# Kernel optimization log

Hardware: AMD Instinct MI355X
Metric: run time of the kernel (lower is better)

## Reference

```python
import jax, jax.numpy as jnp
import numpy as np

B, C, H, W = 4, 128, 192, 192

def _conv(x, w, b, pad):
    y = jax.lax.conv_general_dilated(
        x, w, window_strides=(1, 1), padding=[(pad, pad), (pad, pad)],
        dimension_numbers=('NCHW', 'OIHW', 'NCHW'))
    return y + b[None, :, None, None]

def setup_inputs() -> dict:
    key = jax.random.key(0)
    ks = jax.random.split(key, 11)
    def he(k, shape):
        fan_in = shape[1] * shape[2] * shape[3]
        return jax.random.normal(k, shape, jnp.float32) * np.sqrt(2.0 / fan_in)
    return {
        'x':  jax.random.normal(ks[0], (B, C, H, W), jnp.float32),
        'w1': he(ks[1], (C // 2, C, 3, 3)),      'b1': jnp.zeros((C // 2,), jnp.float32),
        'w2': he(ks[2], (C // 4, C // 2, 3, 3)), 'b2': jnp.zeros((C // 4,), jnp.float32),
        'w3': he(ks[3], (9, C // 4, 1, 1)),      'b3': jnp.zeros((9,), jnp.float32),
        'f1': he(ks[4], (C, C, 3, 3)),           'fb1': jnp.zeros((C,), jnp.float32),
        'f2': he(ks[5], (C, C, 3, 3)),           'fb2': jnp.zeros((C,), jnp.float32),
    }

def reference(x, w1, b1, w2, b2, w3, b3, f1, fb1, f2, fb2):
    b, c, h, w = x.shape
    # kernel estimator: conv3x3 -> relu -> conv3x3 -> relu -> conv1x1 (9 logits)
    k = jax.nn.relu(_conv(x, w1, b1, 1))
    k = jax.nn.relu(_conv(k, w2, b2, 1))
    k = _conv(k, w3, b3, 0)                     # (b, 9, h, w)
    kernel = jax.nn.softmax(k, axis=1)[:, None]  # (b, 1, 9, h, w)
    # 3x3 neighborhoods (equivalent to F.unfold with padding=1), row-major taps
    xp = jnp.pad(x, ((0, 0), (0, 0), (1, 1), (1, 1)))
    patches = jnp.stack([xp[:, :, i:i + h, j:j + w]
                         for i in range(3) for j in range(3)], axis=2)  # (b, c, 9, h, w)
    out = jnp.sum(patches * kernel, axis=2)     # (b, c, h, w)
    # feature extract
    feats = jax.nn.relu(_conv(out, f1, fb1, 1))
    feats = _conv(feats, f2, fb2, 1)
    return feats
```

## Files before the change

### kernel.cpp

```cpp
#include <hip/hip_runtime.h>
#include <math.h>

#define BB 4
#define CC 128
#define HH 192
#define WW 192
#define HWSZ (HH * WW)
#define NPIX (BB * HWSZ)
#define PD 194

typedef __attribute__((ext_vector_type(8))) short short8;
typedef __attribute__((ext_vector_type(4))) short short4v;
typedef __attribute__((ext_vector_type(4))) float float4v;

__device__ __forceinline__ short f2bf(float f) {
    unsigned u = __float_as_uint(f);
    u += 0x7FFF + ((u >> 16) & 1);
    return (short)(u >> 16);
}
__device__ __forceinline__ float bf2f(short s) {
    return __uint_as_float(((unsigned)(unsigned short)s) << 16);
}

__global__ void prep_w_kernel(const float* __restrict__ w,
                              short* __restrict__ wp,
                              int CIN, int COUT, int total) {
    int idx = blockIdx.x * blockDim.x + threadIdx.x;
    if (idx >= total) return;
    int ci8 = idx & 7;
    int t   = idx >> 3;
    int co  = t % COUT;  t /= COUT;
    int lg  = t % 4;     t /= 4;
    int tap3 = t % 3;    t /= 3;
    int tt  = t % 3;
    int ck  = t / 3;
    int cin = ck * 32 + lg * 8 + ci8;
    int tap = tt * 3 + tap3;
    wp[idx] = f2bf(w[(co * CIN + cin) * 9 + tap]);
}

__global__ void zero_pads_kernel(short* __restrict__ p0,
                                 short* __restrict__ p1,
                                 short* __restrict__ p2) {
    int idx = blockIdx.x * blockDim.x + threadIdx.x;
    if (idx >= 3 * 64 * 772) return;
    int e   = idx % 772;
    int bc  = (idx / 772) % 64;
    int buf = idx / (772 * 64);
    short* base = (buf == 0) ? p0 : (buf == 1) ? p1 : p2;
    int row, col;
    if (e < 194)      { row = 0;   col = e; }
    else if (e < 388) { row = 193; col = e - 194; }
    else { int e2 = e - 388; row = 1 + (e2 >> 1); col = (e2 & 1) * 193; }
    short8 z = {0, 0, 0, 0, 0, 0, 0, 0};
    *(short8*)&base[(((size_t)bc * PD + row) * PD + col) * 8] = z;
}

__global__ void x_prep_kernel(const float* __restrict__ x,
                              short* __restrict__ xp) {
    int idx = blockIdx.x * blockDim.x + threadIdx.x;
    if (idx >= BB * 16 * HWSZ) return;
    int w  = idx % WW;
    int h  = (idx / WW) % HH;
    int cg = (idx / HWSZ) % 16;
    int b  = idx / (HWSZ * 16);
    const float* p = x + ((size_t)(b * CC + cg * 8) * HH + h) * WW + w;
    short8 pk;
#pragma unroll
    for (int j = 0; j < 8; ++j) pk[j] = f2bf(p[(size_t)j * HWSZ]);
    *(short8*)&xp[((((size_t)b * 16 + cg) * PD + h + 1) * PD + (w + 1)) * 8] = pk;
}

template <int CIN, int COUT, int WAVES_M, int WAVES_N, int WM, int WN,
          bool RELU, bool OUT_F32>
__global__ __launch_bounds__(WAVES_M * WAVES_N * 64, 4)
void conv3x3_wlds(const short* __restrict__ in,
                  const short* __restrict__ wp,
                  const float* __restrict__ bias,
                  void* __restrict__ outv) {
    constexpr int CKN   = CIN / 32;
    constexpr int CG_IN = CIN / 8;
    constexpr int CGO   = COUT / 8;
    constexpr int NT    = WAVES_M * WAVES_N * 64;
    constexpr int SUB   = 3 * 4 * COUT * 8;
    constexpr int SUBB  = SUB * 2;
    constexpr int ATS   = 4 * COUT * 16;
    constexpr int NS    = CKN * 3;
    constexpr int KTMAX = CKN * 9;
    constexpr int CKB   = PD * PD * 64;
    static_assert(WAVES_M * WM * 16 == COUT, "M tiling");
    static_assert(WAVES_N * WN * 16 == 192, "N tiling");

    __shared__ __align__(16) short s_w[2 * SUB];

    const int tid  = threadIdx.x;
    const int lin  = blockIdx.y * gridDim.x + blockIdx.x;
    const int L    = (lin & 7) * ((HH * BB) >> 3) + (lin >> 3);
    const int h    = L % HH;
    const int b    = L / HH;
    const int lane = tid & 63;
    const int wv   = tid >> 6;
    const int wv_m = wv % WAVES_M;
    const int wv_n = wv / WAVES_M;
    const int ln15 = lane & 15;
    const int lg   = lane >> 4;

    float4v acc[WM][WN];
#pragma unroll
    for (int mi = 0; mi < WM; ++mi)
#pragma unroll
        for (int ni = 0; ni < WN; ++ni)
            acc[mi][ni] = (float4v){0.f, 0.f, 0.f, 0.f};

    short8 Aa[2][WM], Bb[3][WN];

    const int colb = (wv_n * WN * 16 + ln15) * 16;
    const char* rowb0 = (const char*)(in +
        (((size_t)b * CG_IN + lg) * PD + h) * (size_t)PD * 8) + colb;
    const char* rowb1 = rowb0 + PD * 16;
    const char* rowb2 = rowb0 + 2 * PD * 16;

    const char* aBase = (const char*)&s_w[0] +
        lg * (COUT * 16) + (wv_m * WM) * 256 + ln15 * 16;

    auto loadBpf = [&](int dy, int dx, short8* dst) {
        const char* rp = (dy == 0) ? rowb0 : (dy == 1) ? rowb1 : rowb2;
#pragma unroll
        for (int ni = 0; ni < WN; ++ni)
            dst[ni] = *(const short8*)(rp + dx * 16 + ni * 256);
    };

    const short* wsrc = wp;
    int wpar = 0;
    auto stageIssue = [&]() {
        constexpr int UNITS = SUB / 8;
        short* dstb = &s_w[wpar * SUB];
#pragma unroll
        for (int u = 0; u < (UNITS + NT - 1) / NT; ++u) {
            int i = tid + u * NT;
            if (UNITS % NT == 0 || i < UNITS)
                __builtin_amdgcn_global_load_lds(
                    (const __attribute__((address_space(1))) void*)&wsrc[i * 8],
                    (__attribute__((address_space(3))) void*)&dstb[i * 8], 16, 0, 0);
        }
        asm volatile("" ::: "memory");
        wsrc += SUB;
        wpar ^= 1;
    };

    stageIssue();
    loadBpf(0, 0, Bb[0]);
    loadBpf(0, 1, Bb[1]);
    asm volatile("s_waitcnt vmcnt(6)" ::: "memory");
    __builtin_amdgcn_s_barrier();
    asm volatile("" ::: "memory");

    int par = 0;
    for (int ck = 0; ck < CKN; ++ck) {
#pragma unroll
        for (int tt = 0; tt < 3; ++tt) {
            const int s = ck * 3 + tt;
            const bool notLast = (s + 1 < NS);
            if (notLast) stageIssue();
            const char* aP = aBase + (par ? SUBB : 0);
#pragma unroll
            for (int mi = 0; mi < WM; ++mi)
                Aa[0][mi] = *(const short8*)(aP + mi * 256);
#pragma unroll
            for (int t3 = 0; t3 < 3; ++t3) {
                if (t3 < 2) {
#pragma unroll
                    for (int mi = 0; mi < WM; ++mi)
                        Aa[(t3 + 1) & 1][mi] =
                            *(const short8*)(aP + (t3 + 1) * ATS + mi * 256);
                }
                const int kt = s * 3 + t3;
                if (kt + 2 < KTMAX) {
                    const int tp = (tt * 3 + t3 + 2) % 9;
                    loadBpf(tp / 3, tp % 3, Bb[(t3 + 2) % 3]);
                }
#pragma unroll
                for (int mi = 0; mi < WM; ++mi)
#pragma unroll
                    for (int ni = 0; ni < WN; ++ni)
                        acc[mi][ni] = __builtin_amdgcn_mfma_f32_16x16x32_bf16(
                            Aa[t3 & 1][mi], Bb[t3][ni], acc[mi][ni], 0, 0, 0);
                if (tt == 2 && t3 == 0) {
                    rowb0 += CKB; rowb1 += CKB; rowb2 += CKB;
                }
            }
            if (notLast) {
                asm volatile("s_waitcnt vmcnt(9)" ::: "memory");
                __builtin_amdgcn_s_barrier();
                asm volatile("" ::: "memory");
                par ^= 1;
            }
        }
    }

    if (OUT_F32) {
        float* out = (float*)outv;
#pragma unroll
        for (int mi = 0; mi < WM; ++mi) {
            int co0 = (wv_m * WM + mi) * 16 + lg * 4;
#pragma unroll
            for (int r = 0; r < 4; ++r) {
                int co = co0 + r;
                float bv = bias[co];
#pragma unroll
                for (int ni = 0; ni < WN; ++ni) {
                    int wcol = (wv_n * WN + ni) * 16 + ln15;
                    float v = acc[mi][ni][r] + bv;
                    if (RELU) v = fmaxf(v, 0.f);
                    out[((size_t)(b * COUT + co) * HH + h) * WW + wcol] = v;
                }
            }
        }
    } else {
        short* out = (short*)outv;
#pragma unroll
        for (int mi = 0; mi < WM; ++mi) {
            int co0 = (wv_m * WM + mi) * 16 + lg * 4;
            int cg  = co0 >> 3;
            int sub = co0 & 7;
#pragma unroll
            for (int ni = 0; ni < WN; ++ni) {
                int wcol = (wv_n * WN + ni) * 16 + ln15;
                short4v pk;
#pragma unroll
                for (int r = 0; r < 4; ++r) {
                    float v = acc[mi][ni][r] + bias[co0 + r];
                    if (RELU) v = fmaxf(v, 0.f);
                    pk[r] = f2bf(v);
                }
                *(short4v*)&out[((((size_t)b * CGO + cg) * PD + (h + 1)) * PD +
                                 (wcol + 1)) * 8 + sub] = pk;
            }
        }
    }
}

__global__ void conv1x1_softmax_kernel(const short* __restrict__ t2,
                                       const float* __restrict__ w3,
                                       const float* __restrict__ b3,
                                       float* __restrict__ kern) {
    __shared__ float sw[9 * 32];
    __shared__ float sb[9];
    for (int i = threadIdx.x; i < 9 * 32; i += blockDim.x) sw[i] = w3[i];
    if (threadIdx.x < 9) sb[threadIdx.x] = b3[threadIdx.x];
    __syncthreads();

    int idx = blockIdx.x * blockDim.x + threadIdx.x;
    if (idx >= NPIX) return;
    int b = idx / HWSZ;
    int p = idx % HWSZ;
    int h = p / WW, w = p % WW;

    float v[32];
#pragma unroll
    for (int cg = 0; cg < 4; ++cg) {
        short8 pk = *(const short8*)
            &t2[((((size_t)b * 4 + cg) * PD + h + 1) * PD + (w + 1)) * 8];
#pragma unroll
        for (int j = 0; j < 8; ++j) v[cg * 8 + j] = bf2f(pk[j]);
    }

    float lg[9];
    float m = -1e30f;
#pragma unroll
    for (int t = 0; t < 9; ++t) {
        float s = sb[t];
#pragma unroll
        for (int c = 0; c < 32; ++c) s = fmaf(sw[t * 32 + c], v[c], s);
        lg[t] = s;
        m = fmaxf(m, s);
    }
    float sum = 0.f;
#pragma unroll
    for (int t = 0; t < 9; ++t) {
        lg[t] = __expf(lg[t] - m);
        sum += lg[t];
    }
    float inv = 1.f / sum;
#pragma unroll
    for (int t = 0; t < 9; ++t)
        kern[((size_t)(b * 9 + t)) * HWSZ + p] = lg[t] * inv;
}

__global__ void deblur_kernel(const float* __restrict__ x,
                              const float* __restrict__ kern,
                              short* __restrict__ t3) {
    int idx = blockIdx.x * blockDim.x + threadIdx.x;
    if (idx >= BB * 16 * HWSZ) return;
    int w  = idx % WW;
    int h  = (idx / WW) % HH;
    int cg = (idx / HWSZ) % 16;
    int b  = idx / (HWSZ * 16);

    const float* kb = kern + (size_t)(b * 9) * HWSZ + h * WW + w;
    float kv[9];
#pragma unroll
    for (int t = 0; t < 9; ++t) kv[t] = kb[(size_t)t * HWSZ];

    const float* xb = x + (size_t)(b * CC + cg * 8) * HWSZ;
    float s[8] = {0.f, 0.f, 0.f, 0.f, 0.f, 0.f, 0.f, 0.f};
    int t = 0;
#pragma unroll
    for (int dy = 0; dy < 3; ++dy) {
#pragma unroll
        for (int dx = 0; dx < 3; ++dx) {
            int hh = h + dy - 1, ww2 = w + dx - 1;
            if ((unsigned)hh < (unsigned)HH && (unsigned)ww2 < (unsigned)WW) {
                const float* xp = xb + hh * WW + ww2;
#pragma unroll
                for (int j = 0; j < 8; ++j)
                    s[j] = fmaf(kv[t], xp[(size_t)j * HWSZ], s[j]);
            }
            ++t;
        }
    }
    short8 pk;
#pragma unroll
    for (int j = 0; j < 8; ++j) pk[j] = f2bf(s[j]);
    *(short8*)&t3[((((size_t)b * 16 + cg) * PD + h + 1) * PD + (w + 1)) * 8] = pk;
}

extern "C" void kernel_launch(void* const* d_in, const int* in_sizes, int n_in,
                              void* d_out, int out_size, void* d_ws, size_t ws_size,
                              hipStream_t stream) {
    const float* x   = (const float*)d_in[0];
    const float* w1  = (const float*)d_in[1];
    const float* b1  = (const float*)d_in[2];
    const float* w2  = (const float*)d_in[3];
    const float* b2  = (const float*)d_in[4];
    const float* w3  = (const float*)d_in[5];
    const float* b3  = (const float*)d_in[6];
    const float* f1  = (const float*)d_in[7];
    const float* fb1 = (const float*)d_in[8];
    const float* f2  = (const float*)d_in[9];
    const float* fb2 = (const float*)d_in[10];
    float* out = (float*)d_out;

    const size_t ACT_SZ = (size_t)BB * 16 * PD * PD * 8;
    short* xpad    = (short*)d_ws;
    short* regionA = xpad + ACT_SZ;
    short* regionB = regionA + ACT_SZ;
    float* kern    = (float*)(regionB + ACT_SZ);
    short* wp1     = (short*)(kern + (size_t)BB * 9 * HWSZ);
    short* wp2     = wp1 + 9 * 4 * 64 * 32;
    short* wpf1    = wp2 + 9 * 2 * 32 * 32;
    short* wpf2    = wpf1 + 9 * 4 * 128 * 32;

    short* t1 = regionA;
    short* t2 = regionB;
    short* t3 = regionA;
    short* t4 = regionB;

    {
        int nz = 3 * 64 * 772;
        zero_pads_kernel<<<(nz + 255) / 256, 256, 0, stream>>>(xpad, regionA, regionB);
        int nx = BB * 16 * HWSZ;
        x_prep_kernel<<<(nx + 255) / 256, 256, 0, stream>>>(x, xpad);
        int n1 = 9 * 4 * 64 * 32, n2 = 9 * 2 * 32 * 32, nf = 9 * 4 * 128 * 32;
        prep_w_kernel<<<(n1 + 255) / 256, 256, 0, stream>>>(w1, wp1, 128, 64, n1);
        prep_w_kernel<<<(n2 + 255) / 256, 256, 0, stream>>>(w2, wp2, 64, 32, n2);
        prep_w_kernel<<<(nf + 255) / 256, 256, 0, stream>>>(f1, wpf1, 128, 128, nf);
        prep_w_kernel<<<(nf + 255) / 256, 256, 0, stream>>>(f2, wpf2, 128, 128, nf);
    }

    conv3x3_wlds<128, 64, 1, 4, 4, 3, true, false>
        <<<dim3(HH, BB), 256, 0, stream>>>(xpad, wp1, b1, t1);
    conv3x3_wlds<64, 32, 1, 4, 2, 3, true, false>
        <<<dim3(HH, BB), 256, 0, stream>>>(t1, wp2, b2, t2);
    conv1x1_softmax_kernel<<<(NPIX + 255) / 256, 256, 0, stream>>>(t2, w3, b3, kern);
    {
        int nd = BB * 16 * HWSZ;
        deblur_kernel<<<(nd + 255) / 256, 256, 0, stream>>>(x, kern, t3);
    }
    conv3x3_wlds<128, 128, 2, 4, 4, 3, true, false>
        <<<dim3(HH, BB), 512, 0, stream>>>(t3, wpf1, fb1, t4);
    conv3x3_wlds<128, 128, 2, 4, 4, 3, false, true>
        <<<dim3(HH, BB), 512, 0, stream>>>(t4, wpf2, fb2, out);
}
```

Before: 349.2 us.

## Split 128-channel feature convs into two output-channel slices per row

The two 128→128 feature convolutions now launch twice as many 256-thread workgroups, each computing 64 output channels for one image row. Weights are repacked per slice so each workgroup streams only its half into LDS. MFMA blocks are also wrapped in s_setprio to raise wave priority during math. The aim is more, smaller workgroups for better occupancy and latency hiding, at the cost of reading each input row twice.

Result: faster. 330.2 us (-5.4%).

```diff
diff --git a/kernel.cpp b/kernel.cpp
--- a/kernel.cpp
+++ b/kernel.cpp
@@ -24,19 +24,22 @@
 
 __global__ void prep_w_kernel(const float* __restrict__ w,
                               short* __restrict__ wp,
-                              int CIN, int COUT, int total) {
+                              int CIN, int COUT, int NSLICE, int total) {
     int idx = blockIdx.x * blockDim.x + threadIdx.x;
     if (idx >= total) return;
+    int CKN = CIN / 32;
     int ci8 = idx & 7;
     int t   = idx >> 3;
     int co  = t % COUT;  t /= COUT;
     int lg  = t % 4;     t /= 4;
     int tap3 = t % 3;    t /= 3;
-    int tt  = t % 3;
-    int ck  = t / 3;
+    int tt  = t % 3;     t /= 3;
+    int ck  = t % CKN;
+    int sl  = t / CKN;
     int cin = ck * 32 + lg * 8 + ci8;
     int tap = tt * 3 + tap3;
-    wp[idx] = f2bf(w[(co * CIN + cin) * 9 + tap]);
+    int co_g = sl * COUT + co;
+    wp[idx] = f2bf(w[(co_g * CIN + cin) * 9 + tap]);
 }
 
 __global__ void zero_pads_kernel(short* __restrict__ p0,
@@ -71,7 +74,7 @@
     *(short8*)&xp[((((size_t)b * 16 + cg) * PD + h + 1) * PD + (w + 1)) * 8] = pk;
 }
 
-template <int CIN, int COUT, int WAVES_M, int WAVES_N, int WM, int WN,
+template <int CIN, int COUT, int NSLICE, int WAVES_M, int WAVES_N, int WM, int WN,
           bool RELU, bool OUT_F32>
 __global__ __launch_bounds__(WAVES_M * WAVES_N * 64, 4)
 void conv3x3_wlds(const short* __restrict__ in,
@@ -80,7 +83,8 @@
                   void* __restrict__ outv) {
     constexpr int CKN   = CIN / 32;
     constexpr int CG_IN = CIN / 8;
-    constexpr int CGO   = COUT / 8;
+    constexpr int COUT_TOT = COUT * NSLICE;
+    constexpr int CGO   = COUT_TOT / 8;
     constexpr int NT    = WAVES_M * WAVES_N * 64;
     constexpr int SUB   = 3 * 4 * COUT * 8;
     constexpr int SUBB  = SUB * 2;
@@ -88,16 +92,19 @@
     constexpr int NS    = CKN * 3;
     constexpr int KTMAX = CKN * 9;
     constexpr int CKB   = PD * PD * 64;
+    constexpr int WPSL  = NS * SUB;
+    constexpr int NWG   = BB * HH * NSLICE;
     static_assert(WAVES_M * WM * 16 == COUT, "M tiling");
     static_assert(WAVES_N * WN * 16 == 192, "N tiling");
 
     __shared__ __align__(16) short s_w[2 * SUB];
 
     const int tid  = threadIdx.x;
-    const int lin  = blockIdx.y * gridDim.x + blockIdx.x;
-    const int L    = (lin & 7) * ((HH * BB) >> 3) + (lin >> 3);
-    const int h    = L % HH;
-    const int b    = L / HH;
+    const int lin  = blockIdx.y * (HH * NSLICE) + blockIdx.x;
+    const int L    = (lin & 7) * (NWG >> 3) + (lin >> 3);
+    const int sl   = L % NSLICE;
+    const int h    = (L / NSLICE) % HH;
+    const int b    = L / (NSLICE * HH);
     const int lane = tid & 63;
     const int wv   = tid >> 6;
     const int wv_m = wv % WAVES_M;
@@ -130,7 +137,7 @@
             dst[ni] = *(const short8*)(rp + dx * 16 + ni * 256);
     };
 
-    const short* wsrc = wp;
+    const short* wsrc = wp + (size_t)sl * WPSL;
     int wpar = 0;
     auto stageIssue = [&]() {
         constexpr int UNITS = SUB / 8;
@@ -179,12 +186,14 @@
                     const int tp = (tt * 3 + t3 + 2) % 9;
                     loadBpf(tp / 3, tp % 3, Bb[(t3 + 2) % 3]);
                 }
+                __builtin_amdgcn_s_setprio(1);
 #pragma unroll
                 for (int mi = 0; mi < WM; ++mi)
 #pragma unroll
                     for (int ni = 0; ni < WN; ++ni)
                         acc[mi][ni] = __builtin_amdgcn_mfma_f32_16x16x32_bf16(
                             Aa[t3 & 1][mi], Bb[t3][ni], acc[mi][ni], 0, 0, 0);
+                __builtin_amdgcn_s_setprio(0);
                 if (tt == 2 && t3 == 0) {
                     rowb0 += CKB; rowb1 += CKB; rowb2 += CKB;
                 }
@@ -202,7 +211,7 @@
         float* out = (float*)outv;
 #pragma unroll
         for (int mi = 0; mi < WM; ++mi) {
-            int co0 = (wv_m * WM + mi) * 16 + lg * 4;
+            int co0 = sl * COUT + (wv_m * WM + mi) * 16 + lg * 4;
 #pragma unroll
             for (int r = 0; r < 4; ++r) {
                 int co = co0 + r;
@@ -212,7 +221,7 @@
                     int wcol = (wv_n * WN + ni) * 16 + ln15;
                     float v = acc[mi][ni][r] + bv;
                     if (RELU) v = fmaxf(v, 0.f);
-                    out[((size_t)(b * COUT + co) * HH + h) * WW + wcol] = v;
+                    out[((size_t)(b * COUT_TOT + co) * HH + h) * WW + wcol] = v;
                 }
             }
         }
@@ -220,7 +229,7 @@
         short* out = (short*)outv;
 #pragma unroll
         for (int mi = 0; mi < WM; ++mi) {
-            int co0 = (wv_m * WM + mi) * 16 + lg * 4;
+            int co0 = sl * COUT + (wv_m * WM + mi) * 16 + lg * 4;
             int cg  = co0 >> 3;
             int sub = co0 & 7;
 #pragma unroll
@@ -362,23 +371,23 @@
         int nx = BB * 16 * HWSZ;
         x_prep_kernel<<<(nx + 255) / 256, 256, 0, stream>>>(x, xpad);
         int n1 = 9 * 4 * 64 * 32, n2 = 9 * 2 * 32 * 32, nf = 9 * 4 * 128 * 32;
-        prep_w_kernel<<<(n1 + 255) / 256, 256, 0, stream>>>(w1, wp1, 128, 64, n1);
-        prep_w_kernel<<<(n2 + 255) / 256, 256, 0, stream>>>(w2, wp2, 64, 32, n2);
-        prep_w_kernel<<<(nf + 255) / 256, 256, 0, stream>>>(f1, wpf1, 128, 128, nf);
-        prep_w_kernel<<<(nf + 255) / 256, 256, 0, stream>>>(f2, wpf2, 128, 128, nf);
-    }
-
-    conv3x3_wlds<128, 64, 1, 4, 4, 3, true, false>
+        prep_w_kernel<<<(n1 + 255) / 256, 256, 0, stream>>>(w1, wp1, 128, 64, 1, n1);
+        prep_w_kernel<<<(n2 + 255) / 256, 256, 0, stream>>>(w2, wp2, 64, 32, 1, n2);
+        prep_w_kernel<<<(nf + 255) / 256, 256, 0, stream>>>(f1, wpf1, 128, 64, 2, nf);
+        prep_w_kernel<<<(nf + 255) / 256, 256, 0, stream>>>(f2, wpf2, 128, 64, 2, nf);
+    }
+
+    conv3x3_wlds<128, 64, 1, 1, 4, 4, 3, true, false>
         <<<dim3(HH, BB), 256, 0, stream>>>(xpad, wp1, b1, t1);
-    conv3x3_wlds<64, 32, 1, 4, 2, 3, true, false>
+    conv3x3_wlds<64, 32, 1, 1, 4, 2, 3, true, false>
         <<<dim3(HH, BB), 256, 0, stream>>>(t1, wp2, b2, t2);
     conv1x1_softmax_kernel<<<(NPIX + 255) / 256, 256, 0, stream>>>(t2, w3, b3, kern);
     {
         int nd = BB * 16 * HWSZ;
         deblur_kernel<<<(nd + 255) / 256, 256, 0, stream>>>(x, kern, t3);
     }
-    conv3x3_wlds<128, 128, 2, 4, 4, 3, true, false>
-        <<<dim3(HH, BB), 512, 0, stream>>>(t3, wpf1, fb1, t4);
-    conv3x3_wlds<128, 128, 2, 4, 4, 3, false, true>
-        <<<dim3(HH, BB), 512, 0, stream>>>(t4, wpf2, fb2, out);
-}
+    conv3x3_wlds<128, 64, 2, 1, 4, 4, 3, true, false>
+        <<<dim3(HH * 2, BB), 256, 0, stream>>>(t3, wpf1, fb1, t4);
+    conv3x3_wlds<128, 64, 2, 1, 4, 4, 3, false, true>
+        <<<dim3(HH * 2, BB), 256, 0, stream>>>(t4, wpf2, fb2, out);
+}
```
